# Kernel tuning notes

Measured on AMD Instinct MI355X. Metric: run time of the kernel, lower is better.

The kernel has to match this reference:

```python
import jax, jax.numpy as jnp
import numpy as np

NUM_REL = 20000
NUM_EDGES = 640000
DIM_IN = 128
DIM_OUT = 256
NUM_HEAD = 8
DIM_HID = DIM_OUT // NUM_HEAD
NUM_BIN = 10


def setup_inputs() -> dict:
    key = jax.random.key(0)
    ks = jax.random.split(key, 8)
    emb_rel = jax.random.normal(ks[0], (NUM_REL, DIM_IN), dtype=jnp.float32)
    head = jax.random.randint(ks[1], (NUM_EDGES,), 0, NUM_REL)
    tail = jax.random.randint(ks[2], (NUM_EDGES,), 0, NUM_REL)
    bins = jax.random.randint(ks[3], (NUM_EDGES,), 0, NUM_BIN)
    relation_triplets = jnp.stack([head, tail, bins], axis=-1).astype(jnp.int64)
    # parameters (xavier-style scale)
    attn_proj_w = jax.random.normal(ks[4], (DIM_OUT, 2 * DIM_IN), dtype=jnp.float32) * (2.0 / (2 * DIM_IN + DIM_OUT)) ** 0.5
    attn_proj_b = jnp.zeros((DIM_OUT,), dtype=jnp.float32)
    attn_bin = jax.random.normal(ks[5], (NUM_BIN, NUM_HEAD, 1), dtype=jnp.float32) * 0.02
    attn_vec = jax.random.normal(ks[6], (1, NUM_HEAD, DIM_HID), dtype=jnp.float32) * (2.0 / (1 + DIM_HID)) ** 0.5
    aggr_proj_w = jax.random.normal(ks[7], (DIM_OUT, DIM_IN), dtype=jnp.float32) * (2.0 / (DIM_IN + DIM_OUT)) ** 0.5
    aggr_proj_b = jnp.zeros((DIM_OUT,), dtype=jnp.float32)
    return {"emb_rel": emb_rel, "relation_triplets": relation_triplets,
            "attn_proj_w": attn_proj_w, "attn_proj_b": attn_proj_b,
            "attn_bin": attn_bin, "attn_vec": attn_vec,
            "aggr_proj_w": aggr_proj_w, "aggr_proj_b": aggr_proj_b}


def reference(emb_rel, relation_triplets, attn_proj_w, attn_proj_b, attn_bin, attn_vec, aggr_proj_w, aggr_proj_b):
    num_rel = emb_rel.shape[0]
    head = relation_triplets[:, 0]
    tail = relation_triplets[:, 1]
    bins = relation_triplets[:, 2]
    # [E, 2*Din] gather + concat, then attention projection
    concat = jnp.concatenate([emb_rel[head], emb_rel[tail]], axis=-1)
    z = (concat @ attn_proj_w.T + attn_proj_b).reshape(-1, NUM_HEAD, DIM_HID)
    a = jax.nn.leaky_relu(z, negative_slope=0.2)
    # [E, H]: per-head attention logits plus bin bias
    raw = jnp.einsum('ehd,xhd->eh', a, attn_vec) + attn_bin[bins, :, 0]
    # segment softmax over edges grouped by head relation
    amax = jax.ops.segment_max(raw, head, num_segments=num_rel)  # [R, H]
    attn_val = jnp.exp(raw - amax[head])
    sums = jax.ops.segment_sum(attn_val, head, num_segments=num_rel)  # [R, H]
    beta = attn_val / (sums[head] + 1e-16)  # [E, H]
    # weighted aggregation of projected tail embeddings
    msg = (emb_rel[tail] @ aggr_proj_w.T + aggr_proj_b).reshape(-1, NUM_HEAD, DIM_HID)
    out = jax.ops.segment_sum(beta[..., None] * msg, head, num_segments=num_rel)  # [R, H, Dh]
    return out.reshape(num_rel, -1)
```

## Files before the change

### kernel.cpp

```cpp
#include <hip/hip_runtime.h>
#include <hip/hip_fp16.h>
#include <cstdint>
#include <cstddef>

#define NUM_REL 20000
#define NUM_EDGES 640000
#define DIM_IN 128
#define DIM_OUT 256
#define NUM_HEAD 8
#define DIM_HID 32
#define NUM_BIN 10
#define CAP 192


typedef _Float16 f16x8 __attribute__((ext_vector_type(8)));
typedef _Float16 h2 __attribute__((ext_vector_type(2)));
typedef float f32x4 __attribute__((ext_vector_type(4)));

union H2U { unsigned u; h2 h; };

__global__ __launch_bounds__(256) void prep_kernel(
    const float* __restrict__ attn_w, const float* __restrict__ aggr_w,
    __half* __restrict__ Bh, int* __restrict__ cursor) {
  const int b = blockIdx.x, tid = threadIdx.x;
  if (b < 20) {
    int idx = b * 1024 + tid * 4;
    *(int4*)(cursor + idx) = make_int4(0, 0, 0, 0);
    return;
  }
  int i = (b - 20) * 256 + tid;
  int o = (i * 4) >> 7;
  int k = (i * 4) & 127;
  float4 v;
  if (o < 256)      v = *(const float4*)(attn_w + (size_t)o * 256 + k);
  else if (o < 512) v = *(const float4*)(attn_w + (size_t)(o - 256) * 256 + 128 + k);
  else              v = *(const float4*)(aggr_w + (size_t)(o - 512) * 128 + k);
  __half2 h0 = __floats2half2_rn(v.x, v.y);
  __half2 h1 = __floats2half2_rn(v.z, v.w);
  uint2 u;
  u.x = *(unsigned*)&h0;
  u.y = *(unsigned*)&h1;
  *(uint2*)(Bh + (size_t)o * 128 + k) = u;
}

__global__ __launch_bounds__(256) void work_kernel(
    const float* __restrict__ emb, const __half* __restrict__ Bh,
    const float* __restrict__ attn_b, const float* __restrict__ aggr_b,
    __half* __restrict__ P16, const int* __restrict__ trip,
    int* __restrict__ cursor, int* __restrict__ tbsorted) {
  __shared__ float biasF[768];
  const int tid = threadIdx.x;

  if (blockIdx.x >= 1250) {
    int e = (blockIdx.x - 1250) * 256 + tid;
    int hd = trip[e * 3 + 0];
    int tl = trip[e * 3 + 1];
    int bn = trip[e * 3 + 2];
    int pos = atomicAdd(&cursor[hd], 1);
    if (pos < CAP) tbsorted[hd * CAP + pos] = tl | (bn << 15);
    return;
  }

  const int w = tid >> 6, l = tid & 63;
  const int m0 = (blockIdx.x >> 1) * 32;
  const int half_ = blockIdx.x & 1;
  const int lr = l & 15, lk = l >> 4;

  for (int c = tid; c < 768; c += 256) {
    float b = 0.f;
    if (c >= 512)      b = aggr_b[c - 512];
    else if (c >= 256) b = attn_b[c - 256];
    biasF[c] = b;
  }
  __syncthreads();

  f16x8 a[2][4];
  #pragma unroll
  for (int rt = 0; rt < 2; ++rt) {
    const float* src = emb + (size_t)(m0 + rt * 16 + lr) * 128 + lk * 8;
    #pragma unroll
    for (int kt = 0; kt < 4; ++kt) {
      float4 f0 = *(const float4*)(src + kt * 32);
      float4 f1 = *(const float4*)(src + kt * 32 + 4);
      f16x8 v;
      v[0] = (_Float16)f0.x; v[1] = (_Float16)f0.y; v[2] = (_Float16)f0.z; v[3] = (_Float16)f0.w;
      v[4] = (_Float16)f1.x; v[5] = (_Float16)f1.y; v[6] = (_Float16)f1.z; v[7] = (_Float16)f1.w;
      a[rt][kt] = v;
    }
  }

  const int colbase = half_ * 384 + w * 96;
  #pragma unroll 1
  for (int ct = 0; ct < 6; ++ct) {
    const int c0 = colbase + ct * 16;
    const int col = c0 + lr;
    f16x8 bw[4];
    const __half* bsrc = Bh + (size_t)col * 128 + lk * 8;
    #pragma unroll
    for (int kt = 0; kt < 4; ++kt)
      bw[kt] = *reinterpret_cast<const f16x8*>(bsrc + kt * 32);
    f32x4 acc0 = {0.f, 0.f, 0.f, 0.f};
    f32x4 acc1 = {0.f, 0.f, 0.f, 0.f};
    #pragma unroll
    for (int kt = 0; kt < 4; ++kt) {
      acc0 = __builtin_amdgcn_mfma_f32_16x16x32_f16(bw[kt], a[0][kt], acc0, 0, 0, 0);
      acc1 = __builtin_amdgcn_mfma_f32_16x16x32_f16(bw[kt], a[1][kt], acc1, 0, 0, 0);
    }
    const int cq = c0 + lk * 4;
    int d;
    if (cq < 256)      d = cq;
    else if (cq < 512) d = 256 + ((cq - 256) >> 2) * 8;
    else               d = 260 + ((cq - 512) >> 2) * 8;
    float4 bb = *(const float4*)&biasF[cq];
    __half2 h0 = __floats2half2_rn(acc0[0] + bb.x, acc0[1] + bb.y);
    __half2 h1 = __floats2half2_rn(acc0[2] + bb.z, acc0[3] + bb.w);
    uint2 u0; u0.x = *(unsigned*)&h0; u0.y = *(unsigned*)&h1;
    *(uint2*)(P16 + (size_t)(m0 + lr) * 768 + d) = u0;
    h0 = __floats2half2_rn(acc1[0] + bb.x, acc1[1] + bb.y);
    h1 = __floats2half2_rn(acc1[2] + bb.z, acc1[3] + bb.w);
    uint2 u1; u1.x = *(unsigned*)&h0; u1.y = *(unsigned*)&h1;
    *(uint2*)(P16 + (size_t)(m0 + 16 + lr) * 768 + d) = u1;
  }
}

__global__ __launch_bounds__(256) void edge_agg_kernel(
    const __half* __restrict__ P16, const int* __restrict__ tbsorted,
    const int* __restrict__ cursor, const float* __restrict__ attn_bin,
    const float* __restrict__ attn_vec, float* __restrict__ out) {
  __shared__ float binS[NUM_BIN][8];
  const int tid = threadIdx.x;
  if (tid < NUM_BIN * 8) binS[tid >> 3][tid & 7] = attn_bin[tid];
  __syncthreads();

  const int lane = tid & 63;
  const int w = tid >> 6;
  const int r = blockIdx.x * 4 + w;
  const int h = lane >> 3;
  int n = cursor[r];
  n = n < CAP ? n : CAP;
  if (n == 0) {
    *(float4*)(out + (size_t)r * 256 + lane * 4) = make_float4(0.f, 0.f, 0.f, 0.f);
    return;
  }

  float4 vvf = *(const float4*)(attn_vec + lane * 4);
  h2 vv0 = {(_Float16)vvf.x, (_Float16)vvf.y};
  h2 vv1 = {(_Float16)vvf.z, (_Float16)vvf.w};
  const uint2 zhu = *(const uint2*)(P16 + (size_t)r * 768 + lane * 4);
  H2U zh0, zh1; zh0.u = zhu.x; zh1.u = zhu.y;
  const h2 c06 = {(_Float16)0.6f, (_Float16)0.6f};
  const h2 c04 = {(_Float16)0.4f, (_Float16)0.4f};
  const char* base = (const char*)P16;
  const unsigned laneoff = 512u + (unsigned)lane * 16u;
  const int* tbs = tbsorted + r * CAP;

  float s = 0.f;
  float4 acc = make_float4(0.f, 0.f, 0.f, 0.f);

  unsigned tb0 = (unsigned)tbs[0];
  uint4 r0 = *(const uint4*)(base + (tb0 & 0x7fffu) * 1536u + laneoff);
  for (int i = 0; i < n; ++i) {
    unsigned tb1 = 0u;
    uint4 r1 = r0;
    if (i + 1 < n) {
      tb1 = (unsigned)tbs[i + 1];
      r1 = *(const uint4*)(base + (tb1 & 0x7fffu) * 1536u + laneoff);
    }
    int bn = (int)(tb0 >> 15);
    H2U a0, a1; a0.u = r0.x; a1.u = r0.y;
    h2 z0 = zh0.h + a0.h;
    h2 z1 = zh1.h + a1.h;
    H2U b0, b1; b0.h = z0; b1.h = z1;
    b0.u &= 0x7FFF7FFFu; b1.u &= 0x7FFF7FFFu;
    h2 l0 = z0 * c06 + b0.h * c04;
    h2 l1 = z1 * c06 + b1.h * c04;
    float p = __builtin_amdgcn_fdot2(l0, vv0, 0.f, false);
    p = __builtin_amdgcn_fdot2(l1, vv1, p, false);
    p += __shfl_xor(p, 1);
    p += __shfl_xor(p, 2);
    p += __shfl_xor(p, 4);
    float raw = fminf(p + binS[bn][h], 60.f);
    float wv = __expf(raw);
    s += wv;
    float2 g0 = __half22float2(*(const __half2*)&r0.z);
    float2 g1 = __half22float2(*(const __half2*)&r0.w);
    acc.x += wv * g0.x;
    acc.y += wv * g0.y;
    acc.z += wv * g1.x;
    acc.w += wv * g1.y;
    tb0 = tb1; r0 = r1;
  }

  float inv = 1.f / (s + 1e-16f);
  float4 o4 = make_float4(acc.x * inv, acc.y * inv, acc.z * inv, acc.w * inv);
  *(float4*)(out + (size_t)r * 256 + lane * 4) = o4;
}

extern "C" void kernel_launch(void* const* d_in, const int* in_sizes, int n_in,
                              void* d_out, int out_size, void* d_ws, size_t ws_size,
                              hipStream_t stream) {
  const float* emb      = (const float*)d_in[0];
  const int*   trip     = (const int*)d_in[1];
  const float* attn_w   = (const float*)d_in[2];
  const float* attn_b   = (const float*)d_in[3];
  const float* attn_bin = (const float*)d_in[4];
  const float* attn_vec = (const float*)d_in[5];
  const float* aggr_w   = (const float*)d_in[6];
  const float* aggr_b   = (const float*)d_in[7];
  float* out = (float*)d_out;

  __half* P16   = (__half*)d_ws;
  __half* Bh    = P16 + (size_t)NUM_REL * 768;
  int* tbsorted = (int*)(Bh + 768 * 128);
  int* cursor   = tbsorted + (size_t)NUM_REL * CAP;

  hipLaunchKernelGGL(prep_kernel, dim3(116), dim3(256), 0, stream,
                     attn_w, aggr_w, Bh, cursor);
  hipLaunchKernelGGL(work_kernel, dim3(1250 + 2500), dim3(256), 0, stream,
                     emb, Bh, attn_b, aggr_b, P16, trip, cursor, tbsorted);
  hipLaunchKernelGGL(edge_agg_kernel, dim3(NUM_REL / 4), dim3(256), 0, stream,
                     P16, tbsorted, cursor, attn_bin, attn_vec, out);
}
```

Baseline: 229.3 us.

## Split each relation's edge list across four waves with deeper prefetch

The edge aggregation kernel now gives each relation a full block of four waves instead of one wave. The waves interleave over the edge list and prefetch two edges ahead. Partial softmax sums and weighted accumulators are reduced through shared memory before the normalized output is written. This shortens the serial per-relation loop and raises memory-level parallelism. The cost is a 4x larger grid, a block-wide barrier, and shared-memory reduction traffic.

Result: faster. 213.6 us (-6.9%).

```diff
diff --git a/kernel.cpp b/kernel.cpp
--- a/kernel.cpp
+++ b/kernel.cpp
@@ -128,20 +128,22 @@
     const int* __restrict__ cursor, const float* __restrict__ attn_bin,
     const float* __restrict__ attn_vec, float* __restrict__ out) {
   __shared__ float binS[NUM_BIN][8];
+  __shared__ float sS[4][8];
+  __shared__ float accS[4][256];
+  const int r = blockIdx.x;
   const int tid = threadIdx.x;
   if (tid < NUM_BIN * 8) binS[tid >> 3][tid & 7] = attn_bin[tid];
   __syncthreads();
 
-  const int lane = tid & 63;
-  const int w = tid >> 6;
-  const int r = blockIdx.x * 4 + w;
-  const int h = lane >> 3;
   int n = cursor[r];
   n = n < CAP ? n : CAP;
   if (n == 0) {
-    *(float4*)(out + (size_t)r * 256 + lane * 4) = make_float4(0.f, 0.f, 0.f, 0.f);
+    out[(size_t)r * 256 + tid] = 0.f;
     return;
   }
+  const int lane = tid & 63;
+  const int w = tid >> 6;
+  const int h = lane >> 3;
 
   float4 vvf = *(const float4*)(attn_vec + lane * 4);
   h2 vv0 = {(_Float16)vvf.x, (_Float16)vvf.y};
@@ -157,15 +159,22 @@
   float s = 0.f;
   float4 acc = make_float4(0.f, 0.f, 0.f, 0.f);
 
-  unsigned tb0 = (unsigned)tbs[0];
-  uint4 r0 = *(const uint4*)(base + (tb0 & 0x7fffu) * 1536u + laneoff);
-  for (int i = 0; i < n; ++i) {
-    unsigned tb1 = 0u;
-    uint4 r1 = r0;
-    if (i + 1 < n) {
-      tb1 = (unsigned)tbs[i + 1];
-      r1 = *(const uint4*)(base + (tb1 & 0x7fffu) * 1536u + laneoff);
-    }
+  unsigned tb0 = 0u, tb1 = 0u, tb2 = 0u;
+  uint4 r0 = make_uint4(0u, 0u, 0u, 0u), r1 = r0;
+  if (w < n) {
+    tb0 = (unsigned)tbs[w];
+    r0 = *(const uint4*)(base + (tb0 & 0x7fffu) * 1536u + laneoff);
+  }
+  if (w + 4 < n) {
+    tb1 = (unsigned)tbs[w + 4];
+    r1 = *(const uint4*)(base + (tb1 & 0x7fffu) * 1536u + laneoff);
+  }
+  if (w + 8 < n) tb2 = (unsigned)tbs[w + 8];
+
+  for (int i = w; i < n; i += 4) {
+    unsigned tb3 = (i + 12 < n) ? (unsigned)tbs[i + 12] : 0u;
+    uint4 r2 = r0;
+    if (i + 8 < n) r2 = *(const uint4*)(base + (tb2 & 0x7fffu) * 1536u + laneoff);
     int bn = (int)(tb0 >> 15);
     H2U a0, a1; a0.u = r0.x; a1.u = r0.y;
     h2 z0 = zh0.h + a0.h;
@@ -188,12 +197,17 @@
     acc.y += wv * g0.y;
     acc.z += wv * g1.x;
     acc.w += wv * g1.y;
-    tb0 = tb1; r0 = r1;
-  }
-
-  float inv = 1.f / (s + 1e-16f);
-  float4 o4 = make_float4(acc.x * inv, acc.y * inv, acc.z * inv, acc.w * inv);
-  *(float4*)(out + (size_t)r * 256 + lane * 4) = o4;
+    tb0 = tb1; tb1 = tb2; tb2 = tb3; r0 = r1; r1 = r2;
+  }
+
+  if ((lane & 7) == 0) sS[w][h] = s;
+  *(float4*)&accS[w][lane * 4] = acc;
+  __syncthreads();
+
+  const int hh = tid >> 5;
+  float S = sS[0][hh] + sS[1][hh] + sS[2][hh] + sS[3][hh];
+  float o = accS[0][tid] + accS[1][tid] + accS[2][tid] + accS[3][tid];
+  out[(size_t)r * 256 + tid] = o / (S + 1e-16f);
 }
 
 extern "C" void kernel_launch(void* const* d_in, const int* in_sizes, int n_in,
@@ -218,6 +232,6 @@
                      attn_w, aggr_w, Bh, cursor);
   hipLaunchKernelGGL(work_kernel, dim3(1250 + 2500), dim3(256), 0, stream,
                      emb, Bh, attn_b, aggr_b, P16, trip, cursor, tbsorted);
-  hipLaunchKernelGGL(edge_agg_kernel, dim3(NUM_REL / 4), dim3(256), 0, stream,
+  hipLaunchKernelGGL(edge_agg_kernel, dim3(NUM_REL), dim3(256), 0, stream,
                      P16, tbsorted, cursor, attn_bin, attn_vec, out);
 }
```
